# Kernel tuning notes

Hardware: AMD Instinct MI355X
Metric: run time of the kernel (lower is better)

The kernel has to match this reference:

```python
import jax, jax.numpy as jnp
import numpy as np
import math

B, D, C_LEN, Q_LEN = 32, 128, 1024, 256
NEG = -1e30

def setup_inputs() -> dict:
    key = jax.random.key(0)
    ks = jax.random.split(key, 8)
    bound = 1.0 / math.sqrt(D)
    return {
        "C": jax.random.normal(ks[0], (B, D, C_LEN), jnp.float32),
        "Q": jax.random.normal(ks[1], (B, D, Q_LEN), jnp.float32),
        "c_mask": jnp.ones((B, C_LEN), jnp.float32),
        "q_mask": jnp.ones((B, Q_LEN), jnp.float32),
        "W0": jax.random.uniform(ks[2], (3 * D,), jnp.float32, -bound, bound),
        # depthwise conv1d: in=4D groups=4D kernel=5 -> weight (4D, 1, 5)
        "dw_w": jax.random.normal(ks[3], (4 * D, 1, 5), jnp.float32) * math.sqrt(2.0 / 5),
        "dw_b": jnp.zeros((4 * D,), jnp.float32),
        # pointwise conv1d: 4D -> D, kernel 1
        "pw_w": jax.random.normal(ks[4], (D, 4 * D, 1), jnp.float32) * math.sqrt(2.0 / (4 * D)),
        "pw_b": jnp.zeros((D,), jnp.float32),
    }

def reference(C, Q, c_mask, q_mask, W0, dw_w, dw_b, pw_w, pw_b):
    d = W0.shape[0] // 3
    C_t = jnp.swapaxes(C, 1, 2)  # (B, c_len, d)
    Q_t = jnp.swapaxes(Q, 1, 2)  # (B, q_len, d)
    w1, w2, w3 = W0[:d], W0[d:2 * d], W0[2 * d:]
    # Trilinear similarity without materializing (B,c,q,3d):
    # S[b,i,j] = C_t[b,i].w1 + Q_t[b,j].w2 + sum_k C_t[b,i,k]*Q_t[b,j,k]*w3[k]
    S = (jnp.einsum('bik,bjk->bij', C_t * w3, Q_t)
         + (C_t @ w1)[:, :, None] + (Q_t @ w2)[:, None, :])  # (B, c_len, q_len)
    q_m = q_mask[:, None, :]
    c_m = c_mask[:, :, None]
    S_bar = jax.nn.softmax(S * q_m + NEG * (1.0 - q_m), axis=2)
    S_bbar = jax.nn.softmax(S * c_m + NEG * (1.0 - c_m), axis=1)
    A = jnp.einsum('bij,bjk->bik', S_bar, Q_t)                       # (B, c_len, d)
    # bmm(S_bar, S_bbar^T) @ C_t  ==  S_bar @ (S_bbar^T @ C_t)
    Bm = jnp.einsum('bij,bjk->bik', S_bar, jnp.einsum('bij,bik->bjk', S_bbar, C_t))
    out = jnp.concatenate([C_t, A, C_t * A, C_t * Bm], axis=2)       # (B, c_len, 4d)
    x = jnp.swapaxes(out, 1, 2)  # (B, 4d, c_len)
    # depthwise separable conv (eval mode: dropout is identity)
    x = jax.lax.conv_general_dilated(x, dw_w, (1,), [(2, 2)],
                                     dimension_numbers=('NCH', 'OIH', 'NCH'),
                                     feature_group_count=x.shape[1]) + dw_b[None, :, None]
    x = jax.lax.conv_general_dilated(x, pw_w, (1,), [(0, 0)],
                                     dimension_numbers=('NCH', 'OIH', 'NCH')) + pw_b[None, :, None]
    return x  # (B, d, c_len)
```

## Files before the change

### kernel.cpp

```cpp
#include <hip/hip_runtime.h>
#include <math.h>

#define NB 32
#define ND 128
#define NC 1024
#define NQ 256
#define NEGV (-1e30f)

typedef __attribute__((ext_vector_type(8))) __bf16 bf16x8;
typedef __attribute__((ext_vector_type(4))) float f32x4;
typedef __attribute__((ext_vector_type(8))) unsigned short u16x8;
typedef __attribute__((ext_vector_type(4))) unsigned short u16x4;

__device__ inline unsigned short f2bf(float f) {
  unsigned u = __builtin_bit_cast(unsigned, f);
  u += 0x7FFFu + ((u >> 16) & 1u);
  return (unsigned short)(u >> 16);
}
__device__ inline float bf2f(unsigned short u) {
  return __builtin_bit_cast(float, (unsigned)u << 16);
}

__global__ __launch_bounds__(256) void k_pwcvt(const float* __restrict__ pwW, unsigned short* __restrict__ pwB16) {
  int idx = blockIdx.x * 256 + threadIdx.x;
  const float4* src = (const float4*)pwW;
  float4 v0 = src[idx * 2], v1 = src[idx * 2 + 1];
  u16x8 o;
  o[0] = f2bf(v0.x); o[1] = f2bf(v0.y); o[2] = f2bf(v0.z); o[3] = f2bf(v0.w);
  o[4] = f2bf(v1.x); o[5] = f2bf(v1.y); o[6] = f2bf(v1.z); o[7] = f2bf(v1.w);
  ((u16x8*)pwB16)[idx] = o;
}

__global__ __launch_bounds__(256) void k_qprep(const float* __restrict__ Q, const float* __restrict__ W0,
                                               unsigned short* __restrict__ qSwz, unsigned short* __restrict__ qT,
                                               float* __restrict__ qb) {
  __shared__ unsigned short T2[128 * 66];
  __shared__ float w2L[128];
  __shared__ float qbP[4][64];
  int b = blockIdx.y, jc = blockIdx.x, j0 = jc * 64, t = threadIdx.x;
  if (t < 128) w2L[t] = W0[ND + t];
  int d = t >> 1, half = t & 1;
  const float* src = Q + ((size_t)b * ND + d) * NQ + j0 + half * 32;
  unsigned short* qdst = qSwz + ((size_t)b * ND + d) * NQ + jc * 64;
  #pragma unroll
  for (int q = 0; q < 4; ++q) {
    float4 v0 = ((const float4*)src)[q * 2];
    float4 v1 = ((const float4*)src)[q * 2 + 1];
    u16x8 o;
    o[0] = f2bf(v0.x); o[1] = f2bf(v0.y); o[2] = f2bf(v0.z); o[3] = f2bf(v0.w);
    o[4] = f2bf(v1.x); o[5] = f2bf(v1.y); o[6] = f2bf(v1.z); o[7] = f2bf(v1.w);
    *(u16x8*)&T2[d * 66 + half * 32 + q * 8] = o;
    int g = half * 4 + q;
    *(u16x8*)&qdst[(g ^ (d & 7)) * 8] = o;
  }
  __syncthreads();
  {
    int jj = t & 63, dq = t >> 6;
    float s = 0.f;
    #pragma unroll 8
    for (int k = 0; k < 32; ++k) {
      int dd = dq * 32 + k;
      s += bf2f(T2[dd * 66 + jj]) * w2L[dd];
    }
    qbP[dq][jj] = s;
  }
  __syncthreads();
  if (t < 64)
    qb[b * NQ + j0 + t] = qbP[0][t] + qbP[1][t] + qbP[2][t] + qbP[3][t];
  {
    int jj = t >> 2, p = t & 3;
    unsigned short* dst = qT + ((size_t)b * NQ + j0 + jj) * ND;
    #pragma unroll
    for (int q = 0; q < 4; ++q) {
      int g = p * 4 + q;
      u16x8 o;
      #pragma unroll
      for (int e = 0; e < 8; ++e) o[e] = T2[(g * 8 + e) * 66 + jj];
      int sg = (g & 8) | ((g & 7) ^ (jj & 7));
      *(u16x8*)&dst[sg * 8] = o;
    }
  }
}

__global__ __launch_bounds__(256) void k_cprep(const float* __restrict__ C, const float* __restrict__ W0,
                                               unsigned short* __restrict__ cw3T, unsigned short* __restrict__ cSwz,
                                               float* __restrict__ cb) {
  __shared__ unsigned short T2[128 * 66];
  __shared__ float w1L[128], w3L[128];
  __shared__ float cbP[4][64];
  int b = blockIdx.y, i0 = blockIdx.x * 64, t = threadIdx.x;
  if (t < 128) { w1L[t] = W0[t]; w3L[t] = W0[2 * ND + t]; }
  int k = t >> 1, half = t & 1;
  const float* src = C + ((size_t)b * ND + k) * NC + i0 + half * 32;
  unsigned short* cdst = cSwz + ((size_t)b * ND + k) * NC + blockIdx.x * 64;
  #pragma unroll
  for (int q = 0; q < 4; ++q) {
    float4 v0 = ((const float4*)src)[q * 2];
    float4 v1 = ((const float4*)src)[q * 2 + 1];
    u16x8 o;
    o[0] = f2bf(v0.x); o[1] = f2bf(v0.y); o[2] = f2bf(v0.z); o[3] = f2bf(v0.w);
    o[4] = f2bf(v1.x); o[5] = f2bf(v1.y); o[6] = f2bf(v1.z); o[7] = f2bf(v1.w);
    *(u16x8*)&T2[k * 66 + half * 32 + q * 8] = o;
    int g = half * 4 + q;
    *(u16x8*)&cdst[(g ^ (k & 7)) * 8] = o;
  }
  __syncthreads();
  {
    int ii = t & 63, kq = t >> 6;
    float s = 0.f;
    #pragma unroll 8
    for (int kk = 0; kk < 32; ++kk) {
      int dd = kq * 32 + kk;
      s += bf2f(T2[dd * 66 + ii]) * w1L[dd];
    }
    cbP[kq][ii] = s;
  }
  __syncthreads();
  if (t < 64)
    cb[b * NC + i0 + t] = cbP[0][t] + cbP[1][t] + cbP[2][t] + cbP[3][t];
  {
    int ii = t >> 2, p = t & 3;
    unsigned short* dst = cw3T + ((size_t)b * NC + i0 + ii) * ND;
    #pragma unroll
    for (int q = 0; q < 4; ++q) {
      int g = p * 4 + q;
      u16x8 o;
      #pragma unroll
      for (int e = 0; e < 8; ++e)
        o[e] = f2bf(bf2f(T2[(g * 8 + e) * 66 + ii]) * w3L[g * 8 + e]);
      int sg = (g & 8) | ((g & 7) ^ (ii & 7));
      *(u16x8*)&dst[sg * 8] = o;
    }
  }
}

__global__ __launch_bounds__(256) void k_stats(const unsigned short* __restrict__ cw3T,
                                               const unsigned short* __restrict__ qT,
                                               const float* __restrict__ cb, const float* __restrict__ qb,
                                               const float* __restrict__ q_mask, const float* __restrict__ c_mask,
                                               float* __restrict__ rowmax, float* __restrict__ rowsum,
                                               float* __restrict__ colPm, float* __restrict__ colPs) {
  __shared__ float rmP[64][4], rsP[64][4];
  __shared__ float cbL[64], cmL[64], qbL[256], qmL[256];
  int b = blockIdx.y, i0 = blockIdx.x * 64;
  int t = threadIdx.x, w = t >> 6, l = t & 63, h = l >> 4, lr = l & 15;
  int wj = w * 64;
  if (t < 64) { cbL[t] = cb[b * NC + i0 + t]; cmL[t] = c_mask[b * NC + i0 + t]; }
  qbL[t] = qb[b * NQ + t];
  qmL[t] = q_mask[b * NQ + t];
  const unsigned short* Arow = cw3T + ((size_t)b * NC + i0) * ND;
  const unsigned short* Brow = qT + (size_t)b * NQ * ND;
  f32x4 acc[4][4] = {};
  #pragma unroll
  for (int ks = 0; ks < 4; ++ks) {
    int g = ks * 4 + h;
    int off = ((g & 8) | ((g & 7) ^ (lr & 7))) * 8;
    bf16x8 a[4], bq[4];
    #pragma unroll
    for (int mi = 0; mi < 4; ++mi)
      a[mi] = *(const bf16x8*)&Arow[(size_t)(mi * 16 + lr) * ND + off];
    #pragma unroll
    for (int nf = 0; nf < 4; ++nf)
      bq[nf] = *(const bf16x8*)&Brow[(size_t)(wj + nf * 16 + lr) * ND + off];
    #pragma unroll
    for (int mi = 0; mi < 4; ++mi)
      #pragma unroll
      for (int nf = 0; nf < 4; ++nf)
        acc[mi][nf] = __builtin_amdgcn_mfma_f32_16x16x32_bf16(a[mi], bq[nf], acc[mi][nf], 0, 0, 0);
  }
  __syncthreads();
  float qbv[4], qmv[4];
  #pragma unroll
  for (int nf = 0; nf < 4; ++nf) {
    int j = wj + nf * 16 + lr;
    qbv[nf] = qbL[j]; qmv[nf] = qmL[j];
  }
  float rmv[4][4], rsv[4][4];
  #pragma unroll
  for (int mi = 0; mi < 4; ++mi)
    #pragma unroll
    for (int r = 0; r < 4; ++r) { rmv[mi][r] = -3.0e38f; rsv[mi][r] = 0.f; }
  #pragma unroll
  for (int mi = 0; mi < 4; ++mi) {
    #pragma unroll
    for (int r = 0; r < 4; ++r) {
      int row = mi * 16 + h * 4 + r;
      float cbr = cbL[row];
      #pragma unroll
      for (int nf = 0; nf < 4; ++nf) {
        float sv = acc[mi][nf][r] + cbr + qbv[nf];
        acc[mi][nf][r] = sv;
        float vq = sv * qmv[nf] + NEGV * (1.f - qmv[nf]);
        float mn = fmaxf(rmv[mi][r], vq);
        rsv[mi][r] = rsv[mi][r] * __expf(rmv[mi][r] - mn) + __expf(vq - mn);
        rmv[mi][r] = mn;
      }
    }
  }
  #pragma unroll
  for (int off = 1; off < 16; off <<= 1) {
    #pragma unroll
    for (int mi = 0; mi < 4; ++mi)
      #pragma unroll
      for (int r = 0; r < 4; ++r) {
        float mo = __shfl_xor(rmv[mi][r], off);
        float so = __shfl_xor(rsv[mi][r], off);
        float mn = fmaxf(rmv[mi][r], mo);
        rsv[mi][r] = rsv[mi][r] * __expf(rmv[mi][r] - mn) + so * __expf(mo - mn);
        rmv[mi][r] = mn;
      }
  }
  if (lr == 0) {
    #pragma unroll
    for (int mi = 0; mi < 4; ++mi)
      #pragma unroll
      for (int r = 0; r < 4; ++r) {
        rmP[mi * 16 + h * 4 + r][w] = rmv[mi][r];
        rsP[mi * 16 + h * 4 + r][w] = rsv[mi][r];
      }
  }
  float pm[4], ps[4];
  #pragma unroll
  for (int nf = 0; nf < 4; ++nf) { pm[nf] = -3.0e38f; ps[nf] = 0.f; }
  #pragma unroll
  for (int mi = 0; mi < 4; ++mi)
    #pragma unroll
    for (int r = 0; r < 4; ++r) {
      int row = mi * 16 + h * 4 + r;
      float cm = cmL[row];
      float cbias = NEGV * (1.f - cm);
      #pragma unroll
      for (int nf = 0; nf < 4; ++nf) {
        float v = acc[mi][nf][r] * cm + cbias;
        float mn = fmaxf(pm[nf], v);
        ps[nf] = ps[nf] * __expf(pm[nf] - mn) + __expf(v - mn);
        pm[nf] = mn;
      }
    }
  #pragma unroll
  for (int off = 16; off < 64; off <<= 1) {
    #pragma unroll
    for (int nf = 0; nf < 4; ++nf) {
      float mo = __shfl_xor(pm[nf], off);
      float so = __shfl_xor(ps[nf], off);
      float mn = fmaxf(pm[nf], mo);
      ps[nf] = ps[nf] * __expf(pm[nf] - mn) + so * __expf(mo - mn);
      pm[nf] = mn;
    }
  }
  if (h == 0) {
    #pragma unroll
    for (int nf = 0; nf < 4; ++nf) {
      int j = wj + nf * 16 + lr;
      colPm[((size_t)blockIdx.x * NB + b) * NQ + j] = pm[nf];
      colPs[((size_t)blockIdx.x * NB + b) * NQ + j] = ps[nf];
    }
  }
  __syncthreads();
  if (t < 64) {
    float m = rmP[t][0], s = rsP[t][0];
    #pragma unroll
    for (int k = 1; k < 4; ++k) {
      float mo = rmP[t][k], so = rsP[t][k];
      float mn = fmaxf(m, mo);
      s = s * __expf(m - mn) + so * __expf(mo - mn);
      m = mn;
    }
    rowmax[b * NC + i0 + t] = m;
    rowsum[b * NC + i0 + t] = s;
  }
}

__global__ __launch_bounds__(256) void k3c_combine(const float* __restrict__ colPm, const float* __restrict__ colPs,
                                                   float* __restrict__ colmax, float* __restrict__ colsum) {
  int idx = blockIdx.x * 256 + threadIdx.x;
  float m = -3.0e38f, s = 0.f;
  #pragma unroll
  for (int tl = 0; tl < 16; ++tl) {
    float mo = colPm[(size_t)tl * NB * NQ + idx];
    float so = colPs[(size_t)tl * NB * NQ + idx];
    float mn = fmaxf(m, mo);
    s = s * __expf(m - mn) + so * __expf(mo - mn);
    m = mn;
  }
  colmax[idx] = m; colsum[idx] = s;
}

__global__ __launch_bounds__(256) void k4f(const unsigned short* __restrict__ cw3T,
                                           const unsigned short* __restrict__ qT,
                                           const unsigned short* __restrict__ cSwz,
                                           const float* __restrict__ cb, const float* __restrict__ qb,
                                           const float* __restrict__ c_mask,
                                           const float* __restrict__ colmax, const float* __restrict__ colsum,
                                           float* __restrict__ partial) {
  __shared__ unsigned short Pt[2][32 * 72];
  __shared__ float cmxL[32], cinvL[32], qbL2[32];
  int b = blockIdx.y;
  int jt = blockIdx.x & 7, split = blockIdx.x >> 3;
  int j0 = jt * 32;
  int t = threadIdx.x, w = t >> 6, l = t & 63, h = l >> 4, lr = l & 15;
  if (t < 32) {
    cmxL[t] = colmax[b * NQ + j0 + t];
    cinvL[t] = 1.0f / colsum[b * NQ + j0 + t];
    qbL2[t] = qb[b * NQ + j0 + t];
  }
  __syncthreads();
  const unsigned short* Ab = cw3T + (size_t)b * NC * ND;
  const unsigned short* Bb = qT + ((size_t)b * NQ + j0) * ND;
  const unsigned short* Cb2 = cSwz + (size_t)b * ND * NC;
  const float* cbB = cb + b * NC;
  const float* cmB = c_mask + b * NC;
  f32x4 accI[2][2] = {};
  for (int ic8 = 0; ic8 < 8; ++ic8) {
    int ic = split * 512 + ic8 * 64;
    unsigned short* Pbuf = Pt[ic8 & 1];
    f32x4 sA[2] = {};
    #pragma unroll
    for (int ks = 0; ks < 4; ++ks) {
      int g = ks * 4 + h;
      int off = ((g & 8) | ((g & 7) ^ (lr & 7))) * 8;
      bf16x8 av = *(const bf16x8*)&Ab[(size_t)(ic + w * 16 + lr) * ND + off];
      #pragma unroll
      for (int jf = 0; jf < 2; ++jf) {
        bf16x8 bv = *(const bf16x8*)&Bb[(size_t)(jf * 16 + lr) * ND + off];
        sA[jf] = __builtin_amdgcn_mfma_f32_16x16x32_bf16(av, bv, sA[jf], 0, 0, 0);
      }
    }
    float cbv[4], cmv[4];
    #pragma unroll
    for (int r = 0; r < 4; ++r) {
      int i_ = w * 16 + h * 4 + r;
      cbv[r] = cbB[ic + i_];
      cmv[r] = cmB[ic + i_];
    }
    #pragma unroll
    for (int jf = 0; jf < 2; ++jf)
      #pragma unroll
      for (int r = 0; r < 4; ++r) {
        int i_ = w * 16 + h * 4 + r;
        int j_ = jf * 16 + lr;
        float sfull = sA[jf][r] + cbv[r] + qbL2[j_];
        float vc = sfull * cmv[r] + NEGV * (1.f - cmv[r]);
        float p = __expf(vc - cmxL[j_]) * cinvL[j_];
        Pbuf[j_ * 72 + (((i_ >> 3) ^ (j_ & 7)) << 3) + (i_ & 7)] = f2bf(p);
      }
    __syncthreads();
    #pragma unroll
    for (int ks = 0; ks < 2; ++ks) {
      bf16x8 aC[2], bP[2];
      #pragma unroll
      for (int mf = 0; mf < 2; ++mf) {
        int d = w * 32 + mf * 16 + lr;
        aC[mf] = *(const bf16x8*)&Cb2[(size_t)d * NC + ic + (((ks * 4 + h) ^ (lr & 7)) * 8)];
      }
      #pragma unroll
      for (int jf = 0; jf < 2; ++jf) {
        int j_ = jf * 16 + lr;
        bP[jf] = *(const bf16x8*)&Pbuf[j_ * 72 + (((ks * 4 + h) ^ (j_ & 7)) * 8)];
      }
      #pragma unroll
      for (int mf = 0; mf < 2; ++mf)
        #pragma unroll
        for (int jf = 0; jf < 2; ++jf)
          accI[mf][jf] = __builtin_amdgcn_mfma_f32_16x16x32_bf16(aC[mf], bP[jf], accI[mf][jf], 0, 0, 0);
    }
  }
  float* pout = partial + ((size_t)(split * NB + b) * ND) * NQ;
  #pragma unroll
  for (int mf = 0; mf < 2; ++mf)
    #pragma unroll
    for (int jf = 0; jf < 2; ++jf)
      #pragma unroll
      for (int r = 0; r < 4; ++r) {
        int d = w * 32 + mf * 16 + h * 4 + r;
        int j = j0 + jf * 16 + lr;
        pout[(size_t)d * NQ + j] = accI[mf][jf][r];
      }
}

__global__ __launch_bounds__(256) void k4c2(const float* __restrict__ partial,
                                            unsigned short* __restrict__ iSwz) {
  int idx = blockIdx.x * 256 + threadIdx.x;
  const size_t n = (size_t)NB * ND * NQ / 4;
  const float4* p = (const float4*)partial;
  float4 a = p[idx], b4 = p[n + idx];
  u16x4 o;
  o[0] = f2bf(a.x + b4.x);
  o[1] = f2bf(a.y + b4.y);
  o[2] = f2bf(a.z + b4.z);
  o[3] = f2bf(a.w + b4.w);
  int lin = idx * 4;
  int j = lin & 255, dd = (lin >> 8) & 127, bb = lin >> 15;
  int g = (j >> 3) & 7, e0 = j & 7;
  int outoff = ((bb * 128 + dd) << 8) + (j & 192) + ((g ^ (dd & 7)) << 3) + e0;
  *(u16x4*)&iSwz[outoff] = o;
}

__global__ __launch_bounds__(256) void k5f(const unsigned short* __restrict__ cw3T,
                                           const unsigned short* __restrict__ qT,
                                           const unsigned short* __restrict__ qSwz,
                                           const unsigned short* __restrict__ iSwz,
                                           const unsigned short* __restrict__ cSwz,
                                           const float* __restrict__ cb, const float* __restrict__ qb,
                                           const float* __restrict__ q_mask,
                                           const float* __restrict__ rowmax, const float* __restrict__ rowsum,
                                           unsigned short* __restrict__ xB) {
  extern __shared__ char sm[];
  unsigned short* cwA = (unsigned short*)sm;
  unsigned short* PlB = (unsigned short*)(sm + 8192);
  float* As = (float*)sm;
  float* Bs = (float*)(sm + 17024);
  __shared__ float rmL[32], riL[32], cbI[32], qbL[256], qmL[256];
  int b = blockIdx.y, i0 = blockIdx.x * 32;
  int t = threadIdx.x, w = t >> 6, l = t & 63, h = l >> 4, lr = l & 15;
  {
    const unsigned short* src = cw3T + ((size_t)b * NC + i0) * ND;
    #pragma unroll
    for (int k = 0; k < 2; ++k) {
      int u = t + k * 256;
      *(u16x8*)&cwA[u * 8] = *(const u16x8*)(src + u * 8);
    }
  }
  if (t < 32) {
    rmL[t] = rowmax[b * NC + i0 + t];
    riL[t] = 1.0f / rowsum[b * NC + i0 + t];
    cbI[t] = cb[b * NC + i0 + t];
  }
  qbL[t] = qb[b * NQ + t];
  qmL[t] = q_mask[b * NQ + t];
  __syncthreads();

  const unsigned short* qTb = qT + (size_t)b * NQ * ND;
  const unsigned short* qSb = qSwz + (size_t)b * ND * NQ;
  const unsigned short* iSb = iSwz + (size_t)b * ND * NQ;
  f32x4 accA[2][2] = {};
  f32x4 accB[2][2] = {};

  for (int jc = 0; jc < 4; ++jc) {
    int j0 = jc * 64;
    unsigned short* Pl = PlB + (jc & 1) * (32 * 72);
    f32x4 sA[2] = {};
    #pragma unroll
    for (int ks = 0; ks < 4; ++ks) {
      int g = ks * 4 + h;
      int off = ((g & 8) | ((g & 7) ^ (lr & 7))) * 8;
      bf16x8 bv = *(const bf16x8*)&qTb[(size_t)(j0 + w * 16 + lr) * ND + off];
      #pragma unroll
      for (int mi = 0; mi < 2; ++mi) {
        bf16x8 av = *(const bf16x8*)&cwA[(mi * 16 + lr) * 128 + off];
        sA[mi] = __builtin_amdgcn_mfma_f32_16x16x32_bf16(av, bv, sA[mi], 0, 0, 0);
      }
    }
    #pragma unroll
    for (int mi = 0; mi < 2; ++mi)
      #pragma unroll
      for (int r = 0; r < 4; ++r) {
        int i_ = mi * 16 + h * 4 + r;
        int j_ = w * 16 + lr;
        float sfull = sA[mi][r] + cbI[i_] + qbL[j0 + j_];
        float qm = qmL[j0 + j_];
        float vq = sfull * qm + NEGV * (1.f - qm);
        float p = __expf(vq - rmL[i_]) * riL[i_];
        Pl[i_ * 72 + (((j_ >> 3) ^ (i_ & 7)) << 3) + (j_ & 7)] = f2bf(p);
      }
    __syncthreads();
    #pragma unroll
    for (int ks = 0; ks < 2; ++ks) {
      bf16x8 aP[2], bQ[2], bI[2];
      #pragma unroll
      for (int mi = 0; mi < 2; ++mi) {
        int i = mi * 16 + lr;
        int slot = (ks * 4 + h) ^ (i & 7);
        aP[mi] = *(const bf16x8*)&Pl[i * 72 + slot * 8];
      }
      #pragma unroll
      for (int nd = 0; nd < 2; ++nd) {
        int d = w * 32 + nd * 16 + lr;
        int slot = (ks * 4 + h) ^ (d & 7);
        bQ[nd] = *(const bf16x8*)&qSb[(size_t)d * NQ + j0 + slot * 8];
        bI[nd] = *(const bf16x8*)&iSb[(size_t)d * NQ + j0 + slot * 8];
      }
      #pragma unroll
      for (int mi = 0; mi < 2; ++mi)
        #pragma unroll
        for (int nd = 0; nd < 2; ++nd) {
          accA[mi][nd] = __builtin_amdgcn_mfma_f32_16x16x32_bf16(aP[mi], bQ[nd], accA[mi][nd], 0, 0, 0);
          accB[mi][nd] = __builtin_amdgcn_mfma_f32_16x16x32_bf16(aP[mi], bI[nd], accB[mi][nd], 0, 0, 0);
        }
    }
  }
  __syncthreads();
  #pragma unroll
  for (int mi = 0; mi < 2; ++mi)
    #pragma unroll
    for (int nd = 0; nd < 2; ++nd) {
      int d = w * 32 + nd * 16 + lr;
      #pragma unroll
      for (int r = 0; r < 4; ++r) {
        int i = mi * 16 + h * 4 + r;
        As[i * 133 + d] = accA[mi][nd][r];
        Bs[i * 133 + d] = accB[mi][nd][r];
      }
    }
  __syncthreads();
  {
    int i4 = (t & 7) * 4, db = t >> 3;
    const unsigned short* cSb = cSwz + (size_t)b * ND * NC;
    unsigned short* xb = xB + (size_t)b * 4 * ND * NC;
    int ib = i0 + i4;
    #pragma unroll
    for (int p = 0; p < 4; ++p) {
      int d = db + p * 32;
      u16x4 c4b = *(const u16x4*)&cSb[(size_t)d * NC + (ib & ~63) + ((((ib >> 3) & 7) ^ (d & 7)) << 3) + (i4 & 7)];
      float cx[4];
      #pragma unroll
      for (int e = 0; e < 4; ++e) cx[e] = bf2f(c4b[e]);
      float4 a4, b4;
      a4.x = As[(i4 + 0) * 133 + d]; a4.y = As[(i4 + 1) * 133 + d];
      a4.z = As[(i4 + 2) * 133 + d]; a4.w = As[(i4 + 3) * 133 + d];
      b4.x = Bs[(i4 + 0) * 133 + d]; b4.y = Bs[(i4 + 1) * 133 + d];
      b4.z = Bs[(i4 + 2) * 133 + d]; b4.w = Bs[(i4 + 3) * 133 + d];
      u16x4 o1, o2, o3;
      o1[0] = f2bf(a4.x); o1[1] = f2bf(a4.y); o1[2] = f2bf(a4.z); o1[3] = f2bf(a4.w);
      o2[0] = f2bf(cx[0] * a4.x); o2[1] = f2bf(cx[1] * a4.y); o2[2] = f2bf(cx[2] * a4.z); o2[3] = f2bf(cx[3] * a4.w);
      o3[0] = f2bf(cx[0] * b4.x); o3[1] = f2bf(cx[1] * b4.y); o3[2] = f2bf(cx[2] * b4.z); o3[3] = f2bf(cx[3] * b4.w);
      *(u16x4*)&xb[(size_t)(0 * ND + d) * NC + i0 + i4] = c4b;
      *(u16x4*)&xb[(size_t)(1 * ND + d) * NC + i0 + i4] = o1;
      *(u16x4*)&xb[(size_t)(2 * ND + d) * NC + i0 + i4] = o2;
      *(u16x4*)&xb[(size_t)(3 * ND + d) * NC + i0 + i4] = o3;
    }
  }
}

__global__ __launch_bounds__(256) void k6_mfma(const unsigned short* __restrict__ x,
                                               const float* __restrict__ dwW, const float* __restrict__ dwB,
                                               const unsigned short* __restrict__ pwB16,
                                               const float* __restrict__ pwB, float* __restrict__ out) {
  extern __shared__ char sm6[];
  unsigned short* xs = (unsigned short*)sm6;
  unsigned short* x1s = (unsigned short*)(sm6 + 7168);
  unsigned short* pws = (unsigned short*)(sm6 + 11776);
  int b = blockIdx.y, l0 = blockIdx.x * 32;
  int t = threadIdx.x, w = t >> 6, l = t & 63, h = l >> 4, lr = l & 15;
  const unsigned short* xb = x + (size_t)b * 4 * ND * NC;
  f32x4 acc[2][2] = {};
  int cgw = t & 63, lb = w * 8;

  for (int ch = 0; ch < 8; ++ch) {
    int cg0 = ch * 64;
    __syncthreads();
    #pragma unroll
    for (int k = 0; k < 2; ++k) {
      int id2 = t + k * 256;
      if (id2 < 384) {
        int row = id2 / 6, seg = id2 % 6;
        int gl = l0 - 8 + seg * 8;
        u16x8 v = {};
        if ((unsigned)gl <= 1016u)
          v = *(const u16x8*)(xb + (size_t)(cg0 + row) * NC + gl);
        *(u16x8*)&xs[row * 56 + seg * 8] = v;
      }
    }
    #pragma unroll
    for (int k = 0; k < 4; ++k) {
      int id2 = t + k * 256;
      int o = id2 >> 3, s8 = id2 & 7;
      *(u16x8*)&pws[o * 72 + s8 * 8] = *(const u16x8*)(pwB16 + (size_t)o * 512 + cg0 + s8 * 8);
    }
    __syncthreads();
    {
      int gch = cg0 + cgw;
      float bias = dwB[gch];
      float dwv[5];
      #pragma unroll
      for (int tp = 0; tp < 5; ++tp) dwv[tp] = dwW[gch * 5 + tp];
      float f[24];
      #pragma unroll
      for (int s = 0; s < 3; ++s) {
        u16x8 v = *(const u16x8*)&xs[cgw * 56 + lb + s * 8];
        #pragma unroll
        for (int e = 0; e < 8; ++e) f[s * 8 + e] = bf2f(v[e]);
      }
      #pragma unroll
      for (int e = 0; e < 8; ++e) {
        float a = bias;
        #pragma unroll
        for (int tp = 0; tp < 5; ++tp)
          a = fmaf(f[e + 6 + tp], dwv[tp], a);
        x1s[(lb + e) * 72 + cgw] = f2bf(a);
      }
    }
    __syncthreads();
    #pragma unroll
    for (int ks = 0; ks < 2; ++ks) {
      bf16x8 aW[2], bX[2];
      #pragma unroll
      for (int mi = 0; mi < 2; ++mi) {
        int o = w * 32 + mi * 16 + lr;
        aW[mi] = *(const bf16x8*)&pws[o * 72 + ks * 32 + h * 8];
      }
      #pragma unroll
      for (int nf = 0; nf < 2; ++nf) {
        int ll = nf * 16 + lr;
        bX[nf] = *(const bf16x8*)&x1s[ll * 72 + ks * 32 + h * 8];
      }
      #pragma unroll
      for (int mi = 0; mi < 2; ++mi)
        #pragma unroll
        for (int nf = 0; nf < 2; ++nf)
          acc[mi][nf] = __builtin_amdgcn_mfma_f32_16x16x32_bf16(aW[mi], bX[nf], acc[mi][nf], 0, 0, 0);
    }
  }
  #pragma unroll
  for (int mi = 0; mi < 2; ++mi) {
    #pragma unroll
    for (int r = 0; r < 4; ++r) {
      int o = w * 32 + mi * 16 + h * 4 + r;
      float bv = pwB[o];
      #pragma unroll
      for (int nf = 0; nf < 2; ++nf)
        out[((size_t)b * ND + o) * NC + l0 + nf * 16 + lr] = acc[mi][nf][r] + bv;
    }
  }
}

extern "C" void kernel_launch(void* const* d_in, const int* in_sizes, int n_in,
                              void* d_out, int out_size, void* d_ws, size_t ws_size,
                              hipStream_t stream) {
  const float* C = (const float*)d_in[0];
  const float* Q = (const float*)d_in[1];
  const float* c_mask = (const float*)d_in[2];
  const float* q_mask = (const float*)d_in[3];
  const float* W0 = (const float*)d_in[4];
  const float* dwW = (const float*)d_in[5];
  const float* dwB = (const float*)d_in[6];
  const float* pwW = (const float*)d_in[7];
  const float* pwB = (const float*)d_in[8];
  float* out = (float*)d_out;
  float* ws = (float*)d_ws;

  float* rowmax = ws;
  float* rowsum = rowmax + NB * NC;
  float* colmax = rowsum + NB * NC;
  float* colsum = colmax + NB * NQ;
  float* cb = colsum + NB * NQ;
  float* qb = cb + NB * NC;
  float* colPm = qb + NB * NQ;
  float* colPs = colPm + 16 * NB * NQ;
  unsigned short* qSwz = (unsigned short*)(colPs + 16 * NB * NQ);
  unsigned short* qT = qSwz + (size_t)NB * ND * NQ;
  unsigned short* iSwz = qT + (size_t)NB * NQ * ND;
  unsigned short* cw3T = iSwz + (size_t)NB * ND * NQ;
  unsigned short* cSwz = cw3T + (size_t)NB * NC * ND;
  unsigned short* pwB16 = cSwz + (size_t)NB * ND * NC;
  float* partial = (float*)(pwB16 + ND * 512);
  unsigned short* xB = (unsigned short*)(partial + 2 * (size_t)NB * ND * NQ);

  k_pwcvt<<<dim3(32), 256, 0, stream>>>(pwW, pwB16);
  k_qprep<<<dim3(4, NB), 256, 0, stream>>>(Q, W0, qSwz, qT, qb);
  k_cprep<<<dim3(16, NB), 256, 0, stream>>>(C, W0, cw3T, cSwz, cb);
  k_stats<<<dim3(16, NB), 256, 0, stream>>>(cw3T, qT, cb, qb, q_mask, c_mask, rowmax, rowsum, colPm, colPs);
  k3c_combine<<<dim3(NB * NQ / 256), 256, 0, stream>>>(colPm, colPs, colmax, colsum);
  k4f<<<dim3(16, NB), 256, 0, stream>>>(cw3T, qT, cSwz, cb, qb, c_mask, colmax, colsum, partial);
  k4c2<<<dim3(NB * ND * NQ / 4 / 256), 256, 0, stream>>>(partial, iSwz);
  k5f<<<dim3(NC / 32, NB), 256, 34048, stream>>>(cw3T, qT, qSwz, iSwz, cSwz, cb, qb, q_mask, rowmax, rowsum, xB);
  k6_mfma<<<dim3(NC / 32, NB), 256, 30208, stream>>>(xB, dwW, dwB, pwB16, pwB, out);
}
```

Measured before the change: 120.8 us.

## Fold column-stat combine into k4f, shrink k5f LDS, double-buffer k6 conv

The separate column softmax-stat combine kernel is removed, and k4f now merges the 16 partial max/sum values per column itself. k5f reuses one LDS staging buffer for the A and B accumulators in two passes, which halves its dynamic shared memory, and both k4f and k5f get occupancy hints in launch_bounds. The final conv kernel double-buffers its input tile in LDS so the next chunk is fetched while the current one is computed, and it reads pointwise weights straight from global memory instead of staging them. The aim is fewer launches and higher occupancy, at the cost of redundant combine work in k4f, an extra barrier in k5f and uncoalesced global weight loads in k6.

```diff
diff --git a/kernel.cpp b/kernel.cpp
--- a/kernel.cpp
+++ b/kernel.cpp
@@ -271,28 +271,13 @@
   }
 }
 
-__global__ __launch_bounds__(256) void k3c_combine(const float* __restrict__ colPm, const float* __restrict__ colPs,
-                                                   float* __restrict__ colmax, float* __restrict__ colsum) {
-  int idx = blockIdx.x * 256 + threadIdx.x;
-  float m = -3.0e38f, s = 0.f;
-  #pragma unroll
-  for (int tl = 0; tl < 16; ++tl) {
-    float mo = colPm[(size_t)tl * NB * NQ + idx];
-    float so = colPs[(size_t)tl * NB * NQ + idx];
-    float mn = fmaxf(m, mo);
-    s = s * __expf(m - mn) + so * __expf(mo - mn);
-    m = mn;
-  }
-  colmax[idx] = m; colsum[idx] = s;
-}
-
-__global__ __launch_bounds__(256) void k4f(const unsigned short* __restrict__ cw3T,
-                                           const unsigned short* __restrict__ qT,
-                                           const unsigned short* __restrict__ cSwz,
-                                           const float* __restrict__ cb, const float* __restrict__ qb,
-                                           const float* __restrict__ c_mask,
-                                           const float* __restrict__ colmax, const float* __restrict__ colsum,
-                                           float* __restrict__ partial) {
+__global__ __launch_bounds__(256, 8) void k4f(const unsigned short* __restrict__ cw3T,
+                                              const unsigned short* __restrict__ qT,
+                                              const unsigned short* __restrict__ cSwz,
+                                              const float* __restrict__ cb, const float* __restrict__ qb,
+                                              const float* __restrict__ c_mask,
+                                              const float* __restrict__ colPm, const float* __restrict__ colPs,
+                                              float* __restrict__ partial) {
   __shared__ unsigned short Pt[2][32 * 72];
   __shared__ float cmxL[32], cinvL[32], qbL2[32];
   int b = blockIdx.y;
@@ -300,8 +285,17 @@
   int j0 = jt * 32;
   int t = threadIdx.x, w = t >> 6, l = t & 63, h = l >> 4, lr = l & 15;
   if (t < 32) {
-    cmxL[t] = colmax[b * NQ + j0 + t];
-    cinvL[t] = 1.0f / colsum[b * NQ + j0 + t];
+    float m = -3.0e38f, s = 0.f;
+    #pragma unroll
+    for (int tl = 0; tl < 16; ++tl) {
+      float mo = colPm[((size_t)tl * NB + b) * NQ + j0 + t];
+      float so = colPs[((size_t)tl * NB + b) * NQ + j0 + t];
+      float mn = fmaxf(m, mo);
+      s = s * __expf(m - mn) + so * __expf(mo - mn);
+      m = mn;
+    }
+    cmxL[t] = m;
+    cinvL[t] = 1.0f / s;
     qbL2[t] = qb[b * NQ + j0 + t];
   }
   __syncthreads();
@@ -396,20 +390,19 @@
   *(u16x4*)&iSwz[outoff] = o;
 }
 
-__global__ __launch_bounds__(256) void k5f(const unsigned short* __restrict__ cw3T,
-                                           const unsigned short* __restrict__ qT,
-                                           const unsigned short* __restrict__ qSwz,
-                                           const unsigned short* __restrict__ iSwz,
-                                           const unsigned short* __restrict__ cSwz,
-                                           const float* __restrict__ cb, const float* __restrict__ qb,
-                                           const float* __restrict__ q_mask,
-                                           const float* __restrict__ rowmax, const float* __restrict__ rowsum,
-                                           unsigned short* __restrict__ xB) {
+__global__ __launch_bounds__(256, 8) void k5f(const unsigned short* __restrict__ cw3T,
+                                              const unsigned short* __restrict__ qT,
+                                              const unsigned short* __restrict__ qSwz,
+                                              const unsigned short* __restrict__ iSwz,
+                                              const unsigned short* __restrict__ cSwz,
+                                              const float* __restrict__ cb, const float* __restrict__ qb,
+                                              const float* __restrict__ q_mask,
+                                              const float* __restrict__ rowmax, const float* __restrict__ rowsum,
+                                              unsigned short* __restrict__ xB) {
   extern __shared__ char sm[];
   unsigned short* cwA = (unsigned short*)sm;
   unsigned short* PlB = (unsigned short*)(sm + 8192);
   float* As = (float*)sm;
-  float* Bs = (float*)(sm + 17024);
   __shared__ float rmL[32], riL[32], cbI[32], qbL[256], qmL[256];
   int b = blockIdx.y, i0 = blockIdx.x * 32;
   int t = threadIdx.x, w = t >> 6, l = t & 63, h = l >> 4, lr = l & 15;
@@ -496,11 +489,8 @@
     for (int nd = 0; nd < 2; ++nd) {
       int d = w * 32 + nd * 16 + lr;
       #pragma unroll
-      for (int r = 0; r < 4; ++r) {
-        int i = mi * 16 + h * 4 + r;
-        As[i * 133 + d] = accA[mi][nd][r];
-        Bs[i * 133 + d] = accB[mi][nd][r];
-      }
+      for (int r = 0; r < 4; ++r)
+        As[(mi * 16 + h * 4 + r) * 133 + d] = accA[mi][nd][r];
     }
   __syncthreads();
   {
@@ -512,62 +502,78 @@
     for (int p = 0; p < 4; ++p) {
       int d = db + p * 32;
       u16x4 c4b = *(const u16x4*)&cSb[(size_t)d * NC + (ib & ~63) + ((((ib >> 3) & 7) ^ (d & 7)) << 3) + (i4 & 7)];
-      float cx[4];
-      #pragma unroll
-      for (int e = 0; e < 4; ++e) cx[e] = bf2f(c4b[e]);
-      float4 a4, b4;
+      float4 a4;
       a4.x = As[(i4 + 0) * 133 + d]; a4.y = As[(i4 + 1) * 133 + d];
       a4.z = As[(i4 + 2) * 133 + d]; a4.w = As[(i4 + 3) * 133 + d];
-      b4.x = Bs[(i4 + 0) * 133 + d]; b4.y = Bs[(i4 + 1) * 133 + d];
-      b4.z = Bs[(i4 + 2) * 133 + d]; b4.w = Bs[(i4 + 3) * 133 + d];
-      u16x4 o1, o2, o3;
+      u16x4 o1, o2;
       o1[0] = f2bf(a4.x); o1[1] = f2bf(a4.y); o1[2] = f2bf(a4.z); o1[3] = f2bf(a4.w);
-      o2[0] = f2bf(cx[0] * a4.x); o2[1] = f2bf(cx[1] * a4.y); o2[2] = f2bf(cx[2] * a4.z); o2[3] = f2bf(cx[3] * a4.w);
-      o3[0] = f2bf(cx[0] * b4.x); o3[1] = f2bf(cx[1] * b4.y); o3[2] = f2bf(cx[2] * b4.z); o3[3] = f2bf(cx[3] * b4.w);
+      o2[0] = f2bf(bf2f(c4b[0]) * a4.x); o2[1] = f2bf(bf2f(c4b[1]) * a4.y);
+      o2[2] = f2bf(bf2f(c4b[2]) * a4.z); o2[3] = f2bf(bf2f(c4b[3]) * a4.w);
       *(u16x4*)&xb[(size_t)(0 * ND + d) * NC + i0 + i4] = c4b;
       *(u16x4*)&xb[(size_t)(1 * ND + d) * NC + i0 + i4] = o1;
       *(u16x4*)&xb[(size_t)(2 * ND + d) * NC + i0 + i4] = o2;
+    }
+  }
+  __syncthreads();
+  #pragma unroll
+  for (int mi = 0; mi < 2; ++mi)
+    #pragma unroll
+    for (int nd = 0; nd < 2; ++nd) {
+      int d = w * 32 + nd * 16 + lr;
+      #pragma unroll
+      for (int r = 0; r < 4; ++r)
+        As[(mi * 16 + h * 4 + r) * 133 + d] = accB[mi][nd][r];
+    }
+  __syncthreads();
+  {
+    int i4 = (t & 7) * 4, db = t >> 3;
+    const unsigned short* cSb = cSwz + (size_t)b * ND * NC;
+    unsigned short* xb = xB + (size_t)b * 4 * ND * NC;
+    int ib = i0 + i4;
+    #pragma unroll
+    for (int p = 0; p < 4; ++p) {
+      int d = db + p * 32;
+      u16x4 c4b = *(const u16x4*)&cSb[(size_t)d * NC + (ib & ~63) + ((((ib >> 3) & 7) ^ (d & 7)) << 3) + (i4 & 7)];
+      float4 b4;
+      b4.x = As[(i4 + 0) * 133 + d]; b4.y = As[(i4 + 1) * 133 + d];
+      b4.z = As[(i4 + 2) * 133 + d]; b4.w = As[(i4 + 3) * 133 + d];
+      u16x4 o3;
+      o3[0] = f2bf(bf2f(c4b[0]) * b4.x); o3[1] = f2bf(bf2f(c4b[1]) * b4.y);
+      o3[2] = f2bf(bf2f(c4b[2]) * b4.z); o3[3] = f2bf(bf2f(c4b[3]) * b4.w);
       *(u16x4*)&xb[(size_t)(3 * ND + d) * NC + i0 + i4] = o3;
     }
   }
 }
 
-__global__ __launch_bounds__(256) void k6_mfma(const unsigned short* __restrict__ x,
-                                               const float* __restrict__ dwW, const float* __restrict__ dwB,
-                                               const unsigned short* __restrict__ pwB16,
-                                               const float* __restrict__ pwB, float* __restrict__ out) {
-  extern __shared__ char sm6[];
-  unsigned short* xs = (unsigned short*)sm6;
-  unsigned short* x1s = (unsigned short*)(sm6 + 7168);
-  unsigned short* pws = (unsigned short*)(sm6 + 11776);
+__global__ __launch_bounds__(256) void k6f2(const unsigned short* __restrict__ x,
+                                            const float* __restrict__ dwW, const float* __restrict__ dwB,
+                                            const unsigned short* __restrict__ pwB16,
+                                            const float* __restrict__ pwB, float* __restrict__ out) {
+  __shared__ unsigned short xs[2][64 * 56];
+  __shared__ unsigned short x1s[2][32 * 72];
   int b = blockIdx.y, l0 = blockIdx.x * 32;
   int t = threadIdx.x, w = t >> 6, l = t & 63, h = l >> 4, lr = l & 15;
   const unsigned short* xb = x + (size_t)b * 4 * ND * NC;
   f32x4 acc[2][2] = {};
   int cgw = t & 63, lb = w * 8;
 
+  #pragma unroll
+  for (int k = 0; k < 2; ++k) {
+    int id2 = t + k * 256;
+    if (id2 < 384) {
+      int row = id2 / 6, seg = id2 % 6;
+      int gl = l0 - 8 + seg * 8;
+      u16x8 v = {};
+      if ((unsigned)gl <= 1016u)
+        v = *(const u16x8*)(xb + (size_t)row * NC + gl);
+      *(u16x8*)&xs[0][row * 56 + seg * 8] = v;
+    }
+  }
+  __syncthreads();
+
   for (int ch = 0; ch < 8; ++ch) {
+    int cur = ch & 1;
     int cg0 = ch * 64;
-    __syncthreads();
-    #pragma unroll
-    for (int k = 0; k < 2; ++k) {
-      int id2 = t + k * 256;
-      if (id2 < 384) {
-        int row = id2 / 6, seg = id2 % 6;
-        int gl = l0 - 8 + seg * 8;
-        u16x8 v = {};
-        if ((unsigned)gl <= 1016u)
-          v = *(const u16x8*)(xb + (size_t)(cg0 + row) * NC + gl);
-        *(u16x8*)&xs[row * 56 + seg * 8] = v;
-      }
-    }
-    #pragma unroll
-    for (int k = 0; k < 4; ++k) {
-      int id2 = t + k * 256;
-      int o = id2 >> 3, s8 = id2 & 7;
-      *(u16x8*)&pws[o * 72 + s8 * 8] = *(const u16x8*)(pwB16 + (size_t)o * 512 + cg0 + s8 * 8);
-    }
-    __syncthreads();
     {
       int gch = cg0 + cgw;
       float bias = dwB[gch];
@@ -577,7 +583,7 @@
       float f[24];
       #pragma unroll
       for (int s = 0; s < 3; ++s) {
-        u16x8 v = *(const u16x8*)&xs[cgw * 56 + lb + s * 8];
+        u16x8 v = *(const u16x8*)&xs[cur][cgw * 56 + lb + s * 8];
         #pragma unroll
         for (int e = 0; e < 8; ++e) f[s * 8 + e] = bf2f(v[e]);
       }
@@ -587,22 +593,37 @@
         #pragma unroll
         for (int tp = 0; tp < 5; ++tp)
           a = fmaf(f[e + 6 + tp], dwv[tp], a);
-        x1s[(lb + e) * 72 + cgw] = f2bf(a);
+        x1s[cur][(lb + e) * 72 + cgw] = f2bf(a);
+      }
+    }
+    if (ch < 7) {
+      #pragma unroll
+      for (int k = 0; k < 2; ++k) {
+        int id2 = t + k * 256;
+        if (id2 < 384) {
+          int row = id2 / 6, seg = id2 % 6;
+          int gl = l0 - 8 + seg * 8;
+          u16x8 v = {};
+          if ((unsigned)gl <= 1016u)
+            v = *(const u16x8*)(xb + (size_t)(cg0 + 64 + row) * NC + gl);
+          *(u16x8*)&xs[cur ^ 1][row * 56 + seg * 8] = v;
+        }
       }
     }
     __syncthreads();
     #pragma unroll
     for (int ks = 0; ks < 2; ++ks) {
+      int koff = cg0 + (ks * 4 + h) * 8;
       bf16x8 aW[2], bX[2];
       #pragma unroll
       for (int mi = 0; mi < 2; ++mi) {
         int o = w * 32 + mi * 16 + lr;
-        aW[mi] = *(const bf16x8*)&pws[o * 72 + ks * 32 + h * 8];
+        aW[mi] = *(const bf16x8*)&pwB16[(size_t)o * 512 + koff];
       }
       #pragma unroll
       for (int nf = 0; nf < 2; ++nf) {
         int ll = nf * 16 + lr;
-        bX[nf] = *(const bf16x8*)&x1s[ll * 72 + ks * 32 + h * 8];
+        bX[nf] = *(const bf16x8*)&x1s[cur][ll * 72 + (ks * 4 + h) * 8];
       }
       #pragma unroll
       for (int mi = 0; mi < 2; ++mi)
@@ -660,9 +681,8 @@
   k_qprep<<<dim3(4, NB), 256, 0, stream>>>(Q, W0, qSwz, qT, qb);
   k_cprep<<<dim3(16, NB), 256, 0, stream>>>(C, W0, cw3T, cSwz, cb);
   k_stats<<<dim3(16, NB), 256, 0, stream>>>(cw3T, qT, cb, qb, q_mask, c_mask, rowmax, rowsum, colPm, colPs);
-  k3c_combine<<<dim3(NB * NQ / 256), 256, 0, stream>>>(colPm, colPs, colmax, colsum);
-  k4f<<<dim3(16, NB), 256, 0, stream>>>(cw3T, qT, cSwz, cb, qb, c_mask, colmax, colsum, partial);
+  k4f<<<dim3(16, NB), 256, 0, stream>>>(cw3T, qT, cSwz, cb, qb, c_mask, colPm, colPs, partial);
   k4c2<<<dim3(NB * ND * NQ / 4 / 256), 256, 0, stream>>>(partial, iSwz);
-  k5f<<<dim3(NC / 32, NB), 256, 34048, stream>>>(cw3T, qT, qSwz, iSwz, cSwz, cb, qb, q_mask, rowmax, rowsum, xB);
-  k6_mfma<<<dim3(NC / 32, NB), 256, 30208, stream>>>(xB, dwW, dwB, pwB16, pwB, out);
-}
+  k5f<<<dim3(NC / 32, NB), 256, 17408, stream>>>(cw3T, qT, qSwz, iSwz, cSwz, cb, qb, q_mask, rowmax, rowsum, xB);
+  k6f2<<<dim3(NC / 32, NB), 256, 0, stream>>>(xB, dwW, dwB, pwB16, pwB, out);
+}
```

New measurement: 171.6 us. 42.0% more time.
